# Optimization experiments

Hardware: AMD Instinct MI355X
Metric: run time of the kernel (lower is better)

The kernel has to match this reference:

```python
import jax, jax.numpy as jnp
import numpy as np

N, C, H, W = 16, 512, 32, 32
OC = C // 8  # shrink = 8


def setup_inputs() -> dict:
    key = jax.random.key(0)
    ks = jax.random.split(key, 8)
    s = lambda fan: 1.0 / np.sqrt(fan)
    return {
        "tensor": jax.random.normal(ks[0], (N, C, H, W), dtype=jnp.float32),
        "key_w": jax.random.normal(ks[1], (OC, C), dtype=jnp.float32) * s(C),
        "key_b": jax.random.normal(ks[2], (OC,), dtype=jnp.float32) * 0.01,
        "query_w": jax.random.normal(ks[3], (OC, C), dtype=jnp.float32) * s(C),
        "query_b": jax.random.normal(ks[4], (OC,), dtype=jnp.float32) * 0.01,
        "value_w": jax.random.normal(ks[5], (C, C), dtype=jnp.float32) * s(C),
        "value_b": jax.random.normal(ks[6], (C,), dtype=jnp.float32) * 0.01,
        "gamma": jax.random.normal(ks[7], (1,), dtype=jnp.float32),
    }


def reference(tensor, key_w, key_b, query_w, query_b, value_w, value_b, gamma):
    n, c, h, w = tensor.shape
    x = tensor.reshape(n, c, h * w)  # [n, c, hw]
    # 1x1 convs are per-position linear maps over channels
    k = jnp.einsum("oc,ncp->nop", key_w, x) + key_b[None, :, None]      # [n, oc, hw]
    q = jnp.einsum("oc,ncp->nop", query_w, x) + query_b[None, :, None]  # [n, oc, hw]
    v = jnp.einsum("oc,ncp->nop", value_w, x) + value_b[None, :, None]  # [n, c, hw]
    # unscaled attention: softmax over keys (last dim)
    scores = jnp.einsum("ncq,nck->nqk", q, k)  # [n, hw, hw]
    attn = jax.nn.softmax(scores, axis=2)
    o = jnp.einsum("nck,nqk->ncq", v, attn).reshape(n, c, h, w)
    return tensor + o * gamma[0]
```

## Files before the change

### kernel.cpp

```cpp
#include <hip/hip_runtime.h>
#include <hip/hip_bf16.h>

typedef __hip_bfloat16 bf16;
typedef __attribute__((ext_vector_type(8))) short bf16x8;
typedef __attribute__((ext_vector_type(4))) float f32x4;

#define NBATCH 16
#define CCH    512
#define PP     1024
#define OCH    64

__device__ __forceinline__ void gload16(const void* g, void* l) {
  __builtin_amdgcn_global_load_lds(
      (const __attribute__((address_space(1))) void*)g,
      (__attribute__((address_space(3))) void*)l, 16, 0, 0);
}
__device__ __forceinline__ float bf2f(bf16 v) { return __bfloat162float(v); }
__device__ __forceinline__ bf16  f2bf(float v) { return __float2bfloat16(v); }

__device__ __forceinline__ void barrier_plain() {
  asm volatile("" ::: "memory");
  __builtin_amdgcn_s_barrier();
  asm volatile("" ::: "memory");
}
__device__ __forceinline__ void barrier_lgkm0() {
  asm volatile("s_waitcnt lgkmcnt(0)" ::: "memory");
  __builtin_amdgcn_s_barrier();
  asm volatile("" ::: "memory");
}

__global__ __launch_bounds__(256) void prep_transpose_kernel(
    const float* __restrict__ x,
    const float* __restrict__ key_w, const float* __restrict__ key_b,
    const float* __restrict__ query_w, const float* __restrict__ query_b,
    const float* __restrict__ value_w, const float* __restrict__ value_b,
    bf16* __restrict__ xhi, bf16* __restrict__ xlo,
    bf16* __restrict__ wqk_hi, bf16* __restrict__ wqk_lo,
    bf16* __restrict__ wv, float* __restrict__ bias_qk, float* __restrict__ bias_v) {
  __shared__ float tile[64 * 65];
  const int bid = blockIdx.x;
  const int tid = threadIdx.x;
  if (bid < 2048) {
    const int pt = bid & 15, ct = (bid >> 4) & 7, n = bid >> 7;
    const size_t xbase = ((size_t)n * CCH + ct * 64) * PP + pt * 64;
#pragma unroll
    for (int i = 0; i < 4; ++i) {
      const int chunk = i * 256 + tid;
      const int row = chunk >> 4, c4 = chunk & 15;
      const f32x4 v = *(const f32x4*)&x[xbase + (size_t)row * PP + c4 * 4];
#pragma unroll
      for (int m = 0; m < 4; ++m) tile[row * 65 + c4 * 4 + m] = v[m];
    }
    __syncthreads();
    const size_t obase = ((size_t)n * PP + pt * 64) * CCH + ct * 64;
#pragma unroll
    for (int ii = 0; ii < 2; ++ii) {
      const int p = ii * 32 + (tid >> 3);
      const int cu = tid & 7;
      bf16x8 hv, lv;
#pragma unroll
      for (int j = 0; j < 8; ++j) {
        const float f = tile[(cu * 8 + j) * 65 + p];
        const bf16 h = f2bf(f);
        const bf16 lo_ = f2bf(f - bf2f(h));
        short hs, ls;
        __builtin_memcpy(&hs, &h, 2);
        __builtin_memcpy(&ls, &lo_, 2);
        hv[j] = hs;
        lv[j] = ls;
      }
      const size_t oidx = obase + (size_t)p * CCH + cu * 8;
      *(bf16x8*)&xhi[oidx] = hv;
      *(bf16x8*)&xlo[oidx] = lv;
    }
  } else {
    const int t = (bid - 2048) * 256 + tid;
    const int TOT_QK = 128 * 512;
    const int TOT_V  = 512 * 512;
    if (t < TOT_QK) {
      const int m = t >> 9, c = t & 511;
      const float v = (m < 64) ? query_w[m * 512 + c] : key_w[(m - 64) * 512 + c];
      const bf16 hi = f2bf(v);
      wqk_hi[t] = hi;
      wqk_lo[t] = f2bf(v - bf2f(hi));
    } else if (t < TOT_QK + TOT_V) {
      const int u = t - TOT_QK;
      wv[u] = f2bf(value_w[u]);
    } else if (t < TOT_QK + TOT_V + 128) {
      const int m = t - (TOT_QK + TOT_V);
      bias_qk[m] = (m < 64) ? query_b[m] : key_b[m - 64];
    } else if (t < TOT_QK + TOT_V + 128 + 512) {
      const int m = t - (TOT_QK + TOT_V + 128);
      bias_v[m] = value_b[m];
    }
  }
}

__global__ __launch_bounds__(256) void gemm_qkv_kernel(
    const bf16* __restrict__ Whi, const bf16* __restrict__ Wlo,
    const bf16* __restrict__ Wv,
    const bf16* __restrict__ XThi, const bf16* __restrict__ XTlo,
    const float* __restrict__ biasqk, const float* __restrict__ biasv,
    bf16* __restrict__ qhi, bf16* __restrict__ qlo,
    bf16* __restrict__ khi, bf16* __restrict__ klo,
    bf16* __restrict__ Vout) {
  __shared__ __align__(16) bf16 sm[4 * 128 * 64];
  const int tid = threadIdx.x, l = tid & 63, w = tid >> 6;
  const int lrow = l >> 3, lcol = (l & 7) * 8, wr = w >> 1, wc = w & 1;
  const f32x4 z = {0.f, 0.f, 0.f, 0.f};
  f32x4 acc[4][4];
#pragma unroll
  for (int i = 0; i < 4; ++i)
#pragma unroll
    for (int j = 0; j < 4; ++j) acc[i][j] = z;

  if (blockIdx.x < 128) {
    const int id = blockIdx.x;
    const int n0 = (id & 7) * 128, bn = id >> 3;
    const size_t xoff = (size_t)bn * PP * CCH;
    bf16* Ash = sm;
    bf16* Asl = sm + 8192;
    bf16* Bsh = sm + 16384;
    bf16* Bsl = sm + 24576;
    for (int kt = 0; kt < CCH; kt += 64) {
#pragma unroll
      for (int it = 0; it < 4; ++it) {
        const int chunk = w * 4 + it;
        const int ar = chunk * 8 + lrow;
        const int br = n0 + chunk * 8 + lrow;
        gload16(Whi + (size_t)ar * CCH + kt + lcol, &Ash[chunk * 512]);
        gload16(Wlo + (size_t)ar * CCH + kt + lcol, &Asl[chunk * 512]);
        gload16(XThi + xoff + (size_t)br * CCH + kt + lcol, &Bsh[chunk * 512]);
        gload16(XTlo + xoff + (size_t)br * CCH + kt + lcol, &Bsl[chunk * 512]);
      }
      __syncthreads();
#pragma unroll
      for (int kk = 0; kk < 2; ++kk) {
        bf16x8 ah[4], al[4], bh[4], bl[4];
        const int ko = kk * 32 + (l >> 4) * 8;
#pragma unroll
        for (int i = 0; i < 4; ++i) {
          const int r = (wr * 64 + i * 16 + (l & 15)) * 64 + ko;
          ah[i] = *(const bf16x8*)&Ash[r];
          al[i] = *(const bf16x8*)&Asl[r];
        }
#pragma unroll
        for (int j = 0; j < 4; ++j) {
          const int r = (wc * 64 + j * 16 + (l & 15)) * 64 + ko;
          bh[j] = *(const bf16x8*)&Bsh[r];
          bl[j] = *(const bf16x8*)&Bsl[r];
        }
#pragma unroll
        for (int i = 0; i < 4; ++i)
#pragma unroll
          for (int j = 0; j < 4; ++j) {
            acc[i][j] = __builtin_amdgcn_mfma_f32_16x16x32_bf16(ah[i], bh[j], acc[i][j], 0, 0, 0);
            acc[i][j] = __builtin_amdgcn_mfma_f32_16x16x32_bf16(ah[i], bl[j], acc[i][j], 0, 0, 0);
            acc[i][j] = __builtin_amdgcn_mfma_f32_16x16x32_bf16(al[i], bh[j], acc[i][j], 0, 0, 0);
          }
      }
      __syncthreads();
    }
    const size_t qoff = (size_t)bn * PP * OCH;
#pragma unroll
    for (int i = 0; i < 4; ++i)
#pragma unroll
      for (int j = 0; j < 4; ++j)
#pragma unroll
        for (int r = 0; r < 4; ++r) {
          const int m = wr * 64 + i * 16 + (l >> 4) * 4 + r;
          const int p = n0 + wc * 64 + j * 16 + (l & 15);
          const float v = acc[i][j][r] + biasqk[m];
          const bf16 hi = f2bf(v);
          const bf16 lo = f2bf(v - bf2f(hi));
          if (m < 64) {
            qhi[qoff + (size_t)p * OCH + m] = hi;
            qlo[qoff + (size_t)p * OCH + m] = lo;
          } else {
            khi[qoff + (size_t)p * OCH + (m - 64)] = hi;
            klo[qoff + (size_t)p * OCH + (m - 64)] = lo;
          }
        }
  } else {
    const int id = blockIdx.x - 128;
    const int n0 = (id & 7) * 128, m0 = ((id >> 3) & 3) * 128, bn = id >> 5;
    const size_t xoff = (size_t)bn * PP * CCH;
    bf16* As = sm;
    bf16* Bs = sm + 8192;
    for (int kt = 0; kt < CCH; kt += 64) {
#pragma unroll
      for (int it = 0; it < 4; ++it) {
        const int chunk = w * 4 + it;
        gload16(Wv + (size_t)(m0 + chunk * 8 + lrow) * CCH + kt + lcol, &As[chunk * 512]);
        gload16(XThi + xoff + (size_t)(n0 + chunk * 8 + lrow) * CCH + kt + lcol, &Bs[chunk * 512]);
      }
      __syncthreads();
#pragma unroll
      for (int kk = 0; kk < 2; ++kk) {
        bf16x8 a[4], b[4];
        const int ko = kk * 32 + (l >> 4) * 8;
#pragma unroll
        for (int i = 0; i < 4; ++i) a[i] = *(const bf16x8*)&As[(wr * 64 + i * 16 + (l & 15)) * 64 + ko];
#pragma unroll
        for (int j = 0; j < 4; ++j) b[j] = *(const bf16x8*)&Bs[(wc * 64 + j * 16 + (l & 15)) * 64 + ko];
#pragma unroll
        for (int i = 0; i < 4; ++i)
#pragma unroll
          for (int j = 0; j < 4; ++j)
            acc[i][j] = __builtin_amdgcn_mfma_f32_16x16x32_bf16(a[i], b[j], acc[i][j], 0, 0, 0);
      }
      __syncthreads();
    }
#pragma unroll
    for (int i = 0; i < 4; ++i)
#pragma unroll
      for (int j = 0; j < 4; ++j)
#pragma unroll
        for (int r = 0; r < 4; ++r) {
          const int m = m0 + wr * 64 + i * 16 + (l >> 4) * 4 + r;
          const int p = n0 + wc * 64 + j * 16 + (l & 15);
          Vout[(size_t)bn * CCH * PP + (size_t)m * PP + p] = f2bf(acc[i][j][r] + biasv[m]);
        }
  }
}

#define NTT 16

__global__ __launch_bounds__(1024, 4) void fused_attn_kernel(
    const bf16* __restrict__ qhi, const bf16* __restrict__ qlo,
    const bf16* __restrict__ khi, const bf16* __restrict__ klo,
    const bf16* __restrict__ vbuf, const float* __restrict__ tensor,
    const float* __restrict__ gamma, float* __restrict__ out) {
  __shared__ __align__(16) char smem[40960];
  __shared__ float red[256];
  __shared__ float fq[64];
  const int tid = threadIdx.x, l = tid & 63, w = tid >> 6;
  const int li = l & 15, g = l >> 4;

  const int d = blockIdx.x;
  const int idx = d >> 3;
  const int bn = (d & 7) * 2 + (idx >> 4);
  const int qt0 = (idx & 15) * 64;

  const size_t qkoff = (size_t)bn * PP * OCH;
  const size_t voff  = (size_t)bn * CCH * PP;
  const int qf = w & 3, kf = (w >> 2) & 3;
  char* Pb = smem + 32768;

  bf16x8 qa_h[2], qa_l[2];
  {
    const int qrow = qt0 + qf * 16 + li;
#pragma unroll
    for (int h = 0; h < 2; ++h) {
      qa_h[h] = *(const bf16x8*)(qhi + qkoff + (size_t)qrow * OCH + h * 32 + g * 8);
      qa_l[h] = *(const bf16x8*)(qlo + qkoff + (size_t)qrow * OCH + h * 32 + g * 8);
    }
  }

  auto stage_k = [&](int t, int buf) {
    char* base = smem + ((w >= 8) ? 16384 : 0) + buf * 8192;
    const bf16* src0 = (w < 8) ? khi : klo;
    const int row = (w & 7) * 8 + (l >> 3);
    const int lu = (l & 7) ^ (row & 7);
    gload16(src0 + qkoff + (size_t)(t * 64 + row) * OCH + lu * 8,
            base + (w & 7) * 1024);
  };

  stage_k(0, 0);
  asm volatile("s_waitcnt vmcnt(0)" ::: "memory");
  __builtin_amdgcn_s_barrier();
  asm volatile("" ::: "memory");

  f32x4 acc[2][4];
  const f32x4 z = {0.f, 0.f, 0.f, 0.f};
#pragma unroll
  for (int i = 0; i < 2; ++i)
#pragma unroll
    for (int j = 0; j < 4; ++j) acc[i][j] = z;
  float psum[4] = {0.f, 0.f, 0.f, 0.f};

  for (int t = 0; t < NTT; ++t) {
    const int buf = t & 1;
    if (t) barrier_plain();

    if (t + 1 < NTT) stage_k(t + 1, buf ^ 1);

    bf16x8 va[2][2];
#pragma unroll
    for (int i = 0; i < 2; ++i)
#pragma unroll
      for (int kc = 0; kc < 2; ++kc)
        va[i][kc] = *(const bf16x8*)(vbuf + voff +
                        (size_t)(w * 32 + i * 16 + li) * PP + t * 64 + kc * 32 + g * 8);

    char* Kh = smem + buf * 8192;
    char* Kl = smem + 16384 + buf * 8192;
    const int krow = kf * 16 + li;
    f32x4 sA = z, sB = z;
#pragma unroll
    for (int h = 0; h < 2; ++h) {
      const int pu = (h * 4 + g) ^ (krow & 7);
      const bf16x8 kh_ = *(const bf16x8*)(Kh + krow * 128 + pu * 16);
      const bf16x8 kl_ = *(const bf16x8*)(Kl + krow * 128 + pu * 16);
      sA = __builtin_amdgcn_mfma_f32_16x16x32_bf16(qa_h[h], kh_, sA, 0, 0, 0);
      sB = __builtin_amdgcn_mfma_f32_16x16x32_bf16(qa_l[h], kh_, sB, 0, 0, 0);
      sB = __builtin_amdgcn_mfma_f32_16x16x32_bf16(qa_h[h], kl_, sB, 0, 0, 0);
    }

#pragma unroll
    for (int r = 0; r < 4; ++r) {
      const float pv = __expf(sA[r] + sB[r] - 30.f);
      const bf16 pb16 = f2bf(pv);
      psum[r] += bf2f(pb16);
      const int q = qf * 16 + g * 4 + r;
      const int k = kf * 16 + li;
      const int pu = (k >> 3) ^ (q & 7);
      *(bf16*)(Pb + q * 128 + pu * 16 + (k & 7) * 2) = pb16;
    }
    barrier_lgkm0();

#pragma unroll
    for (int kc = 0; kc < 2; ++kc) {
      bf16x8 pb[4];
#pragma unroll
      for (int j = 0; j < 4; ++j) {
        const int prow = j * 16 + li;
        const int pu = (kc * 4 + g) ^ (prow & 7);
        pb[j] = *(const bf16x8*)(Pb + prow * 128 + pu * 16);
      }
      __builtin_amdgcn_s_setprio(1);
#pragma unroll
      for (int i = 0; i < 2; ++i)
#pragma unroll
        for (int j = 0; j < 4; ++j)
          acc[i][j] = __builtin_amdgcn_mfma_f32_16x16x32_bf16(va[i][kc], pb[j], acc[i][j], 0, 0, 0);
      __builtin_amdgcn_s_setprio(0);
    }
  }

#pragma unroll
  for (int off = 1; off < 16; off <<= 1)
#pragma unroll
    for (int r = 0; r < 4; ++r) psum[r] += __shfl_xor(psum[r], off);
  if (li == 0) {
#pragma unroll
    for (int r = 0; r < 4; ++r) red[(qf * 16 + g * 4 + r) * 4 + kf] = psum[r];
  }
  __syncthreads();
  if (tid < 64)
    fq[tid] = gamma[0] / (red[tid * 4] + red[tid * 4 + 1] + red[tid * 4 + 2] + red[tid * 4 + 3]);
  __syncthreads();

  float* rep = (float*)smem;
  const size_t obase = (size_t)bn * CCH * PP + qt0;
#pragma unroll
  for (int chunk = 0; chunk < 4; ++chunk) {
    if ((w >> 2) == chunk) {
#pragma unroll
      for (int i = 0; i < 2; ++i)
#pragma unroll
        for (int j = 0; j < 4; ++j) {
          const int q = (j << 4) + li;
          const float f = fq[q];
          const int c0 = ((w & 3) << 5) + (i << 4) + (g << 2);
#pragma unroll
          for (int r = 0; r < 4; ++r) rep[(c0 + r) * 68 + q] = acc[i][j][r] * f;
        }
    }
    __syncthreads();
#pragma unroll
    for (int it = 0; it < 2; ++it) {
      const int cp = it * 1024 + tid, cl = cp >> 4, q4 = cp & 15;
      const size_t gi = obase + (size_t)(chunk * 128 + cl) * PP + q4 * 4;
      const f32x4 tv = *(const f32x4*)&tensor[gi];
      const f32x4 rv = *(const f32x4*)&rep[cl * 68 + q4 * 4];
      *(f32x4*)&out[gi] = tv + rv;
    }
    __syncthreads();
  }
}

extern "C" void kernel_launch(void* const* d_in, const int* in_sizes, int n_in,
                              void* d_out, int out_size, void* d_ws, size_t ws_size,
                              hipStream_t stream) {
  const float* tensor  = (const float*)d_in[0];
  const float* key_w   = (const float*)d_in[1];
  const float* key_b   = (const float*)d_in[2];
  const float* query_w = (const float*)d_in[3];
  const float* query_b = (const float*)d_in[4];
  const float* value_w = (const float*)d_in[5];
  const float* value_b = (const float*)d_in[6];
  const float* gamma   = (const float*)d_in[7];

  char* ws = (char*)d_ws;
  size_t off = 0;
  auto alloc = [&](size_t bytes) -> char* {
    char* p = ws + off;
    off += (bytes + 255) & ~(size_t)255;
    return p;
  };
  bf16* xt_hi  = (bf16*)alloc((size_t)NBATCH * PP * CCH * 2);
  bf16* xt_lo  = (bf16*)alloc((size_t)NBATCH * PP * CCH * 2);
  bf16* wqk_hi = (bf16*)alloc(128 * 512 * 2);
  bf16* wqk_lo = (bf16*)alloc(128 * 512 * 2);
  bf16* wv     = (bf16*)alloc(512 * 512 * 2);
  float* bias_qk = (float*)alloc(128 * 4);
  float* bias_v  = (float*)alloc(512 * 4);
  bf16* q_hi = (bf16*)alloc((size_t)NBATCH * PP * OCH * 2);
  bf16* q_lo = (bf16*)alloc((size_t)NBATCH * PP * OCH * 2);
  bf16* k_hi = (bf16*)alloc((size_t)NBATCH * PP * OCH * 2);
  bf16* k_lo = (bf16*)alloc((size_t)NBATCH * PP * OCH * 2);
  bf16* vbuf = (bf16*)alloc((size_t)NBATCH * CCH * PP * 2);
  (void)ws_size; (void)in_sizes; (void)n_in; (void)out_size;

  prep_transpose_kernel<<<dim3(3331), dim3(256), 0, stream>>>(
      tensor, key_w, key_b, query_w, query_b, value_w, value_b,
      xt_hi, xt_lo, wqk_hi, wqk_lo, wv, bias_qk, bias_v);

  gemm_qkv_kernel<<<dim3(640), dim3(256), 0, stream>>>(
      wqk_hi, wqk_lo, wv, xt_hi, xt_lo, bias_qk, bias_v,
      q_hi, q_lo, k_hi, k_lo, vbuf);

  fused_attn_kernel<<<dim3(256), dim3(1024), 0, stream>>>(
      q_hi, q_lo, k_hi, k_lo, vbuf, tensor, gamma, (float*)d_out);
}
```

Measured before the change: 106.0 us.

## Halve attention block to 512 threads with 32-key tiles and larger per-wave accumulators

Blocks of the fused attention kernel shrink from 16 waves to 8, and each wave now accumulates 64 channels instead of 32, so acc grows to 4x4 tiles. The key tile shrinks from 64 to 32 with 32 iterations, which halves shared memory for K and P and uses a new swizzle for the 64-byte P rows. Barriers now wait on vmcnt before syncing, and V loads are issued ahead of the next K stage. The aim is more register reuse of P fragments and less per-iteration sync overhead, at the cost of more registers per thread and more loop iterations.

```diff
diff --git a/kernel.cpp b/kernel.cpp
--- a/kernel.cpp
+++ b/kernel.cpp
@@ -18,8 +18,8 @@
 __device__ __forceinline__ float bf2f(bf16 v) { return __bfloat162float(v); }
 __device__ __forceinline__ bf16  f2bf(float v) { return __float2bfloat16(v); }
 
-__device__ __forceinline__ void barrier_plain() {
-  asm volatile("" ::: "memory");
+__device__ __forceinline__ void barrier_vm0() {
+  asm volatile("s_waitcnt vmcnt(0)" ::: "memory");
   __builtin_amdgcn_s_barrier();
   asm volatile("" ::: "memory");
 }
@@ -224,15 +224,16 @@
   }
 }
 
-#define NTT 16
-
-__global__ __launch_bounds__(1024, 4) void fused_attn_kernel(
+#define KT 32
+#define NT 32
+
+__global__ __launch_bounds__(512, 4) void fused_attn_kernel(
     const bf16* __restrict__ qhi, const bf16* __restrict__ qlo,
     const bf16* __restrict__ khi, const bf16* __restrict__ klo,
     const bf16* __restrict__ vbuf, const float* __restrict__ tensor,
     const float* __restrict__ gamma, float* __restrict__ out) {
-  __shared__ __align__(16) char smem[40960];
-  __shared__ float red[256];
+  __shared__ __align__(16) char smem[36864];
+  __shared__ float red[128];
   __shared__ float fq[64];
   const int tid = threadIdx.x, l = tid & 63, w = tid >> 6;
   const int li = l & 15, g = l >> 4;
@@ -244,98 +245,96 @@
 
   const size_t qkoff = (size_t)bn * PP * OCH;
   const size_t voff  = (size_t)bn * CCH * PP;
-  const int qf = w & 3, kf = (w >> 2) & 3;
-  char* Pb = smem + 32768;
-
-  bf16x8 qa_h[2], qa_l[2];
+  const int qf = w & 3, kf = w >> 2;
+  char* Pb = smem + 16384;
+
+  bf16x8 ah[2], al[2];
   {
     const int qrow = qt0 + qf * 16 + li;
 #pragma unroll
     for (int h = 0; h < 2; ++h) {
-      qa_h[h] = *(const bf16x8*)(qhi + qkoff + (size_t)qrow * OCH + h * 32 + g * 8);
-      qa_l[h] = *(const bf16x8*)(qlo + qkoff + (size_t)qrow * OCH + h * 32 + g * 8);
+      ah[h] = *(const bf16x8*)(qhi + qkoff + (size_t)qrow * OCH + h * 32 + g * 8);
+      al[h] = *(const bf16x8*)(qlo + qkoff + (size_t)qrow * OCH + h * 32 + g * 8);
     }
   }
 
   auto stage_k = [&](int t, int buf) {
-    char* base = smem + ((w >= 8) ? 16384 : 0) + buf * 8192;
-    const bf16* src0 = (w < 8) ? khi : klo;
-    const int row = (w & 7) * 8 + (l >> 3);
-    const int lu = (l & 7) ^ (row & 7);
-    gload16(src0 + qkoff + (size_t)(t * 64 + row) * OCH + lu * 8,
-            base + (w & 7) * 1024);
+    char* base = smem + ((w >= 4) ? 8192 : 0) + buf * 4096;
+    const bf16* src0 = (w < 4) ? khi : klo;
+    const int s = ((w & 3) << 6) | l;
+    const int row = s >> 3, pu = s & 7, lu = pu ^ (row & 7);
+    gload16(src0 + qkoff + (size_t)(t * KT + row) * OCH + lu * 8,
+            base + (w & 3) * 1024);
   };
 
   stage_k(0, 0);
-  asm volatile("s_waitcnt vmcnt(0)" ::: "memory");
-  __builtin_amdgcn_s_barrier();
-  asm volatile("" ::: "memory");
-
-  f32x4 acc[2][4];
+
+  f32x4 acc[4][4];
   const f32x4 z = {0.f, 0.f, 0.f, 0.f};
 #pragma unroll
-  for (int i = 0; i < 2; ++i)
+  for (int i = 0; i < 4; ++i)
 #pragma unroll
     for (int j = 0; j < 4; ++j) acc[i][j] = z;
   float psum[4] = {0.f, 0.f, 0.f, 0.f};
 
-  for (int t = 0; t < NTT; ++t) {
+  for (int t = 0; t < NT; ++t) {
     const int buf = t & 1;
-    if (t) barrier_plain();
-
-    if (t + 1 < NTT) stage_k(t + 1, buf ^ 1);
-
-    bf16x8 va[2][2];
-#pragma unroll
-    for (int i = 0; i < 2; ++i)
-#pragma unroll
-      for (int kc = 0; kc < 2; ++kc)
-        va[i][kc] = *(const bf16x8*)(vbuf + voff +
-                        (size_t)(w * 32 + i * 16 + li) * PP + t * 64 + kc * 32 + g * 8);
-
-    char* Kh = smem + buf * 8192;
-    char* Kl = smem + 16384 + buf * 8192;
-    const int krow = kf * 16 + li;
-    f32x4 sA = z, sB = z;
+    barrier_vm0();
+
+    bf16x8 va[4];
+#pragma unroll
+    for (int i = 0; i < 4; ++i)
+      va[i] = *(const bf16x8*)(vbuf + voff +
+                  (size_t)(w * 64 + i * 16 + li) * PP + t * KT + g * 8);
+
+    if (t + 1 < NT) stage_k(t + 1, buf ^ 1);
+
+    char* Kh = smem + buf * 4096;
+    char* Kl = smem + 8192 + buf * 4096;
+    bf16x8 kh_[2], kl_[2];
+    const int krow = (kf << 4) + li;
 #pragma unroll
     for (int h = 0; h < 2; ++h) {
-      const int pu = (h * 4 + g) ^ (krow & 7);
-      const bf16x8 kh_ = *(const bf16x8*)(Kh + krow * 128 + pu * 16);
-      const bf16x8 kl_ = *(const bf16x8*)(Kl + krow * 128 + pu * 16);
-      sA = __builtin_amdgcn_mfma_f32_16x16x32_bf16(qa_h[h], kh_, sA, 0, 0, 0);
-      sB = __builtin_amdgcn_mfma_f32_16x16x32_bf16(qa_l[h], kh_, sB, 0, 0, 0);
-      sB = __builtin_amdgcn_mfma_f32_16x16x32_bf16(qa_h[h], kl_, sB, 0, 0, 0);
-    }
+      const int pu = (g + 4 * h) ^ (krow & 7);
+      kh_[h] = *(const bf16x8*)(Kh + krow * 128 + pu * 16);
+      kl_[h] = *(const bf16x8*)(Kl + krow * 128 + pu * 16);
+    }
+    __builtin_amdgcn_s_setprio(1);
+    f32x4 s0 = z, s1 = z, s2 = z;
+    s0 = __builtin_amdgcn_mfma_f32_16x16x32_bf16(ah[0], kh_[0], s0, 0, 0, 0);
+    s1 = __builtin_amdgcn_mfma_f32_16x16x32_bf16(al[0], kh_[0], s1, 0, 0, 0);
+    s2 = __builtin_amdgcn_mfma_f32_16x16x32_bf16(ah[0], kl_[0], s2, 0, 0, 0);
+    s0 = __builtin_amdgcn_mfma_f32_16x16x32_bf16(ah[1], kh_[1], s0, 0, 0, 0);
+    s1 = __builtin_amdgcn_mfma_f32_16x16x32_bf16(al[1], kh_[1], s1, 0, 0, 0);
+    s2 = __builtin_amdgcn_mfma_f32_16x16x32_bf16(ah[1], kl_[1], s2, 0, 0, 0);
+    __builtin_amdgcn_s_setprio(0);
 
 #pragma unroll
     for (int r = 0; r < 4; ++r) {
-      const float pv = __expf(sA[r] + sB[r] - 30.f);
+      const float pv = __expf(s0[r] + s1[r] + s2[r] - 30.f);
       const bf16 pb16 = f2bf(pv);
       psum[r] += bf2f(pb16);
       const int q = qf * 16 + g * 4 + r;
-      const int k = kf * 16 + li;
-      const int pu = (k >> 3) ^ (q & 7);
-      *(bf16*)(Pb + q * 128 + pu * 16 + (k & 7) * 2) = pb16;
+      const int k = (kf << 4) + li;
+      const int pu = (k >> 3) ^ ((q >> 1) & 3);
+      *(bf16*)(Pb + q * 64 + pu * 16 + (k & 7) * 2) = pb16;
     }
     barrier_lgkm0();
 
-#pragma unroll
-    for (int kc = 0; kc < 2; ++kc) {
-      bf16x8 pb[4];
-#pragma unroll
-      for (int j = 0; j < 4; ++j) {
-        const int prow = j * 16 + li;
-        const int pu = (kc * 4 + g) ^ (prow & 7);
-        pb[j] = *(const bf16x8*)(Pb + prow * 128 + pu * 16);
-      }
-      __builtin_amdgcn_s_setprio(1);
-#pragma unroll
-      for (int i = 0; i < 2; ++i)
-#pragma unroll
-        for (int j = 0; j < 4; ++j)
-          acc[i][j] = __builtin_amdgcn_mfma_f32_16x16x32_bf16(va[i][kc], pb[j], acc[i][j], 0, 0, 0);
-      __builtin_amdgcn_s_setprio(0);
-    }
+    bf16x8 pb[4];
+#pragma unroll
+    for (int j = 0; j < 4; ++j) {
+      const int prow = (j << 4) + li;
+      const int pu = g ^ ((prow >> 1) & 3);
+      pb[j] = *(const bf16x8*)(Pb + prow * 64 + pu * 16);
+    }
+    __builtin_amdgcn_s_setprio(1);
+#pragma unroll
+    for (int i = 0; i < 4; ++i)
+#pragma unroll
+      for (int j = 0; j < 4; ++j)
+        acc[i][j] = __builtin_amdgcn_mfma_f32_16x16x32_bf16(va[i], pb[j], acc[i][j], 0, 0, 0);
+    __builtin_amdgcn_s_setprio(0);
   }
 
 #pragma unroll
@@ -344,33 +343,35 @@
     for (int r = 0; r < 4; ++r) psum[r] += __shfl_xor(psum[r], off);
   if (li == 0) {
 #pragma unroll
-    for (int r = 0; r < 4; ++r) red[(qf * 16 + g * 4 + r) * 4 + kf] = psum[r];
+    for (int r = 0; r < 4; ++r) {
+      const int q = qf * 16 + g * 4 + r;
+      red[q * 2 + kf] = psum[r];
+    }
   }
   __syncthreads();
-  if (tid < 64)
-    fq[tid] = gamma[0] / (red[tid * 4] + red[tid * 4 + 1] + red[tid * 4 + 2] + red[tid * 4 + 3]);
+  if (tid < 64) fq[tid] = gamma[0] / (red[tid * 2] + red[tid * 2 + 1]);
   __syncthreads();
 
   float* rep = (float*)smem;
   const size_t obase = (size_t)bn * CCH * PP + qt0;
 #pragma unroll
   for (int chunk = 0; chunk < 4; ++chunk) {
-    if ((w >> 2) == chunk) {
-#pragma unroll
-      for (int i = 0; i < 2; ++i)
+    if ((w >> 1) == chunk) {
+#pragma unroll
+      for (int i = 0; i < 4; ++i)
 #pragma unroll
         for (int j = 0; j < 4; ++j) {
           const int q = (j << 4) + li;
           const float f = fq[q];
-          const int c0 = ((w & 3) << 5) + (i << 4) + (g << 2);
+          const int c0 = ((w & 1) << 6) + (i << 4) + (g << 2);
 #pragma unroll
           for (int r = 0; r < 4; ++r) rep[(c0 + r) * 68 + q] = acc[i][j][r] * f;
         }
     }
     __syncthreads();
 #pragma unroll
-    for (int it = 0; it < 2; ++it) {
-      const int cp = it * 1024 + tid, cl = cp >> 4, q4 = cp & 15;
+    for (int it = 0; it < 4; ++it) {
+      const int cp = it * 512 + tid, cl = cp >> 4, q4 = cp & 15;
       const size_t gi = obase + (size_t)(chunk * 128 + cl) * PP + q4 * 4;
       const f32x4 tv = *(const f32x4*)&tensor[gi];
       const f32x4 rv = *(const f32x4*)&rep[cl * 68 + q4 * 4];
@@ -421,6 +422,6 @@
       wqk_hi, wqk_lo, wv, xt_hi, xt_lo, bias_qk, bias_v,
       q_hi, q_lo, k_hi, k_lo, vbuf);
 
-  fused_attn_kernel<<<dim3(256), dim3(1024), 0, stream>>>(
+  fused_attn_kernel<<<dim3(256), dim3(512), 0, stream>>>(
       q_hi, q_lo, k_hi, k_lo, vbuf, tensor, gamma, (float*)d_out);
 }
```

Result: slower. 137.1 us (+29.4%).
